# Kernel tuning notes

Hardware: AMD Instinct MI355X
Metric: run time of the kernel (lower is better)

The kernel has to match this reference:

```python
import jax, jax.numpy as jnp
import numpy as np

B, N, C = 2048, 49, 768
MID = 48  # 768 // 16
SELECT_SIZES = (36, 24)  # int(49*0.75), int(49*0.5)
LN_EPS = 1e-5


def _hier_se(x, w1, b1, w2, b2):
    """HierarchicalSE: SE gating + importance scores. x: [B, N, C]."""
    s = x.mean(axis=1)  # [B, C]
    h = jax.nn.gelu(s @ w1 + b1, approximate=False)
    gates = jax.nn.sigmoid(h @ w2 + b2)[:, None, :]  # [B, 1, C]
    out = x * gates
    ts = jnp.linalg.norm(out, axis=-1)  # [B, N]
    ts = ts - ts.mean(axis=-1, keepdims=True)
    std = jnp.std(ts, axis=-1, ddof=1, keepdims=True) + 1e-6  # torch std is unbiased
    importance = jax.nn.softmax(ts / std, axis=-1)
    return out, importance


def _select_patches(tokens, importance, k):
    _, idx = jax.lax.top_k(importance, k)  # [B, k]
    return jnp.take_along_axis(tokens, idx[:, :, None], axis=1)  # [B, k, C]


def setup_inputs() -> dict:
    key = jax.random.key(0)
    ks = jax.random.split(key, 8)
    sc = 0.02
    return {
        "x": jax.random.normal(ks[0], (B, N, C), dtype=jnp.float32),
        "se1_w1": jax.random.normal(ks[1], (C, MID), dtype=jnp.float32) * sc,
        "se1_b1": jnp.zeros((MID,), jnp.float32),
        "se1_w2": jax.random.normal(ks[2], (MID, C), dtype=jnp.float32) * sc,
        "se1_b2": jnp.zeros((C,), jnp.float32),
        "se2_w1": jax.random.normal(ks[3], (C, MID), dtype=jnp.float32) * sc,
        "se2_b1": jnp.zeros((MID,), jnp.float32),
        "se2_w2": jax.random.normal(ks[4], (MID, C), dtype=jnp.float32) * sc,
        "se2_b2": jnp.zeros((C,), jnp.float32),
        "ln_gamma": jnp.ones((C,), jnp.float32),
        "ln_beta": jnp.zeros((C,), jnp.float32),
        "cls_w": jax.random.normal(ks[5], (C, 5), dtype=jnp.float32) * sc,
        "cls_b": jnp.zeros((5,), jnp.float32),
    }


def reference(x, se1_w1, se1_b1, se1_w2, se1_b2,
              se2_w1, se2_b1, se2_w2, se2_b2,
              ln_gamma, ln_beta, cls_w, cls_b):
    tokens = x
    params = ((se1_w1, se1_b1, se1_w2, se1_b2), (se2_w1, se2_b1, se2_w2, se2_b2))
    for (w1, b1, w2, b2), k in zip(params, SELECT_SIZES):
        tokens_attn, importance = _hier_se(tokens, w1, b1, w2, b2)
        tokens = _select_patches(tokens_attn, importance, k)
    pooled = tokens.mean(axis=1)  # [B, C]
    mu = pooled.mean(axis=-1, keepdims=True)
    var = pooled.var(axis=-1, keepdims=True)
    normed = (pooled - mu) * jax.lax.rsqrt(var + LN_EPS) * ln_gamma + ln_beta
    return normed @ cls_w + cls_b  # [B, 5]
```

## Files before the change

kernel.cpp:

```cpp
#include <hip/hip_runtime.h>
#include <math.h>

#define NB    2048
#define NTOK  49
#define CH    768
#define MID   48
#define K1    36
#define K2    24
#define NU1   (NTOK - K1)
#define NU2   (K1 - K2)
#define NTHR  384

__device__ __forceinline__ float wsum(float v) {
    #pragma unroll
    for (int off = 32; off; off >>= 1) v += __shfl_xor(v, off, 64);
    return v;
}
__device__ __forceinline__ float gelu_exact(float v) {
    return 0.5f * v * (1.0f + erff(v * 0.70710678118654752440f));
}
__device__ __forceinline__ float sigmoidf(float v) {
    return 1.0f / (1.0f + expf(-v));
}

__global__ __launch_bounds__(NTHR, 6)
void fused_all(const float* __restrict__ x,
               const float* __restrict__ w1a, const float* __restrict__ b1a,
               const float* __restrict__ w2a, const float* __restrict__ b2a,
               const float* __restrict__ w1b, const float* __restrict__ b1b,
               const float* __restrict__ w2b, const float* __restrict__ b2b,
               const float* __restrict__ lng, const float* __restrict__ lnb,
               const float* __restrict__ cw,  const float* __restrict__ cb,
               float* __restrict__ out)
{
    __shared__ float colsum[CH];
    __shared__ float sA[CH];
    __shared__ float gv[CH];
    __shared__ float red[8 * MID];
    __shared__ float hb[MID];
    __shared__ float ts[64];
    __shared__ int   sel1[K1];
    __shared__ int   unsel1[NU1];
    __shared__ int   unsel2[NU2];
    __shared__ float scal[2];

    const int tid  = threadIdx.x;
    const int lane = tid & 63;
    const int wv   = tid >> 6;
    const int b    = blockIdx.x;
    const float* xb = x + (size_t)b * (NTOK * CH);

    {
        const float2* p = (const float2*)xb;
        float sx = 0.f, sy = 0.f;
        #pragma unroll 7
        for (int n = 0; n < NTOK; ++n) {
            float2 v = p[n * 384 + tid];
            sx += v.x; sy += v.y;
        }
        colsum[2*tid]   = sx;
        colsum[2*tid+1] = sy;
    }
    __syncthreads();

    {
        const int m = tid % MID, ch = tid / MID;
        const float* wp = w1a + (ch * 96) * MID + m;
        const float* sp = colsum + ch * 96;
        float a = 0.f;
        #pragma unroll
        for (int k = 0; k < 96; ++k) a = fmaf(sp[k], wp[k * MID], a);
        red[ch * MID + m] = a;
    }
    __syncthreads();
    if (tid < MID) {
        float v = 0.f;
        #pragma unroll
        for (int c = 0; c < 8; ++c) v += red[c * MID + tid];
        hb[tid] = gelu_exact(v * (1.0f / NTOK) + b1a[tid]);
    }
    __syncthreads();

    {
        const float2* w2r = (const float2*)w2a;
        float2 bb = ((const float2*)b2a)[tid];
        float a0 = bb.x, a1 = bb.y;
        #pragma unroll
        for (int m = 0; m < MID; ++m) {
            float2 w = w2r[(size_t)m * 384 + tid];
            float h = hb[m];
            a0 = fmaf(h, w.x, a0);
            a1 = fmaf(h, w.y, a1);
        }
        gv[2*tid]   = sigmoidf(a0);
        gv[2*tid+1] = sigmoidf(a1);
    }
    __syncthreads();

    {
        float gs[12];
        #pragma unroll
        for (int k = 0; k < 3; ++k) {
            float4 q = *(const float4*)&gv[4*lane + 256*k];
            gs[4*k+0] = q.x*q.x; gs[4*k+1] = q.y*q.y;
            gs[4*k+2] = q.z*q.z; gs[4*k+3] = q.w*q.w;
        }
        for (int n = wv; n < NTOK; n += 6) {
            const float4* row = (const float4*)(xb + n * CH);
            float acc = 0.f;
            #pragma unroll
            for (int k = 0; k < 3; ++k) {
                float4 v = row[lane + 64*k];
                acc = fmaf(v.x*v.x, gs[4*k+0], acc);
                acc = fmaf(v.y*v.y, gs[4*k+1], acc);
                acc = fmaf(v.z*v.z, gs[4*k+2], acc);
                acc = fmaf(v.w*v.w, gs[4*k+3], acc);
            }
            acc = wsum(acc);
            if (lane == 0) ts[n] = sqrtf(acc);
        }
    }
    __syncthreads();

    if (wv == 0) {
        float vl = (lane < NTOK) ? ts[lane] : -1.0f;
        int rank = 0;
        for (int j = 0; j < NTOK; ++j) {
            float vj = ts[j];
            rank += (vj > vl) || (vj == vl && j < lane);
        }
        if (lane < NTOK) {
            if (rank < K1) sel1[rank] = lane;
            else           unsel1[rank - K1] = lane;
        }
    }
    __syncthreads();

    {
        int rows[NU1];
        #pragma unroll
        for (int r = 0; r < NU1; ++r) rows[r] = unsel1[r] * CH;
        float2 cs = *(float2*)&colsum[2*tid];
        #pragma unroll
        for (int r = 0; r < NU1; ++r) {
            float2 v = *(const float2*)(xb + rows[r] + 2*tid);
            cs.x -= v.x; cs.y -= v.y;
        }
        *(float2*)&colsum[2*tid] = cs;
        float2 g = *(float2*)&gv[2*tid];
        sA[2*tid]   = cs.x * (1.0f / K1) * g.x;
        sA[2*tid+1] = cs.y * (1.0f / K1) * g.y;
    }
    __syncthreads();

    {
        const int m = tid % MID, ch = tid / MID;
        const float* wp = w1b + (ch * 96) * MID + m;
        const float* sp = sA + ch * 96;
        float a = 0.f;
        #pragma unroll
        for (int k = 0; k < 96; ++k) a = fmaf(sp[k], wp[k * MID], a);
        red[ch * MID + m] = a;
    }
    __syncthreads();
    if (tid < MID) {
        float v = 0.f;
        #pragma unroll
        for (int c = 0; c < 8; ++c) v += red[c * MID + tid];
        hb[tid] = gelu_exact(v + b1b[tid]);
    }
    __syncthreads();

    {
        const float2* w2r = (const float2*)w2b;
        float2 bb = ((const float2*)b2b)[tid];
        float a0 = bb.x, a1 = bb.y;
        #pragma unroll
        for (int m = 0; m < MID; ++m) {
            float2 w = w2r[(size_t)m * 384 + tid];
            float h = hb[m];
            a0 = fmaf(h, w.x, a0);
            a1 = fmaf(h, w.y, a1);
        }
        gv[2*tid]   *= sigmoidf(a0);
        gv[2*tid+1] *= sigmoidf(a1);
    }
    __syncthreads();

    {
        float gr[12];
        #pragma unroll
        for (int k = 0; k < 3; ++k) {
            float4 q = *(const float4*)&gv[4*lane + 256*k];
            gr[4*k+0] = q.x*q.x; gr[4*k+1] = q.y*q.y;
            gr[4*k+2] = q.z*q.z; gr[4*k+3] = q.w*q.w;
        }
        for (int j = wv; j < K1; j += 6) {
            const float4* row = (const float4*)(xb + sel1[j] * CH);
            float acc = 0.f;
            #pragma unroll
            for (int k = 0; k < 3; ++k) {
                float4 v = row[lane + 64*k];
                acc = fmaf(v.x*v.x, gr[4*k+0], acc);
                acc = fmaf(v.y*v.y, gr[4*k+1], acc);
                acc = fmaf(v.z*v.z, gr[4*k+2], acc);
                acc = fmaf(v.w*v.w, gr[4*k+3], acc);
            }
            acc = wsum(acc);
            if (lane == 0) ts[j] = sqrtf(acc);
        }
    }
    __syncthreads();

    if (wv == 0) {
        float vl = (lane < K1) ? ts[lane] : -1.0f;
        int rank = 0;
        for (int j = 0; j < K1; ++j) {
            float vj = ts[j];
            rank += (vj > vl) || (vj == vl && j < lane);
        }
        if (lane < K1 && rank >= K2) unsel2[rank - K2] = sel1[lane];
    }
    __syncthreads();

    {
        int rows[NU2];
        #pragma unroll
        for (int r = 0; r < NU2; ++r) rows[r] = unsel2[r] * CH;
        float2 cs = *(float2*)&colsum[2*tid];
        #pragma unroll
        for (int r = 0; r < NU2; ++r) {
            float2 v = *(const float2*)(xb + rows[r] + 2*tid);
            cs.x -= v.x; cs.y -= v.y;
        }
        float2 g = *(float2*)&gv[2*tid];
        sA[2*tid]   = cs.x * (1.0f / K2) * g.x;
        sA[2*tid+1] = cs.y * (1.0f / K2) * g.y;
    }
    __syncthreads();

    if (wv == 0) {
        float s = 0.f, q = 0.f;
        #pragma unroll
        for (int k = 0; k < CH/64; ++k) {
            float v = sA[lane + 64*k];
            s += v; q = fmaf(v, v, q);
        }
        s = wsum(s); q = wsum(q);
        if (lane == 0) {
            float mu  = s * (1.0f / CH);
            float var = q * (1.0f / CH) - mu * mu;
            scal[0] = mu;
            scal[1] = rsqrtf(var + 1e-5f);
        }
    }
    __syncthreads();

    if (wv < 5) {
        const float mu = scal[0], inv = scal[1];
        float acc = 0.f;
        #pragma unroll
        for (int k = 0; k < CH/64; ++k) {
            int c = lane + 64*k;
            float nv = (sA[c] - mu) * inv * lng[c] + lnb[c];
            acc = fmaf(nv, cw[c*5 + wv], acc);
        }
        acc = wsum(acc);
        if (lane == 0) out[(size_t)b*5 + wv] = acc + cb[wv];
    }
}

extern "C" void kernel_launch(void* const* d_in, const int* in_sizes, int n_in,
                              void* d_out, int out_size, void* d_ws, size_t ws_size,
                              hipStream_t stream) {
    (void)in_sizes; (void)n_in; (void)out_size; (void)d_ws; (void)ws_size;
    const float* x   = (const float*)d_in[0];
    const float* w1a = (const float*)d_in[1];
    const float* b1a = (const float*)d_in[2];
    const float* w2a = (const float*)d_in[3];
    const float* b2a = (const float*)d_in[4];
    const float* w1b = (const float*)d_in[5];
    const float* b1b = (const float*)d_in[6];
    const float* w2b = (const float*)d_in[7];
    const float* b2b = (const float*)d_in[8];
    const float* lng = (const float*)d_in[9];
    const float* lnb = (const float*)d_in[10];
    const float* cw  = (const float*)d_in[11];
    const float* cb  = (const float*)d_in[12];
    float* out = (float*)d_out;

    hipLaunchKernelGGL(fused_all, dim3(NB), dim3(NTHR), 0, stream,
                       x, w1a, b1a, w2a, b2a, w1b, b1b, w2b, b2b,
                       lng, lnb, cw, cb, out);
}
```

Before: 546.0 us.

## Process two batch rows per block to share SE weight loads

Each block now handles two batch elements instead of one. The SE MLP weight reads (w1, w2) are shared across both rows, and the reduction and top-k phases for the two rows run on separate waves. This halves the block count to 1024 and lowers the launch-bounds occupancy target from 6 to 4, which reduces latency hiding for the memory-bound x streaming while cutting redundant weight traffic and per-block sync overhead.

Measured after the change: 527.3 us. -3.4%, faster.

```diff
diff --git a/kernel.cpp b/kernel.cpp
--- a/kernel.cpp
+++ b/kernel.cpp
@@ -10,6 +10,7 @@
 #define NU1   (NTOK - K1)
 #define NU2   (K1 - K2)
 #define NTHR  384
+#define BPB   2
 
 __device__ __forceinline__ float wsum(float v) {
     #pragma unroll
@@ -23,85 +24,98 @@
     return 1.0f / (1.0f + expf(-v));
 }
 
-__global__ __launch_bounds__(NTHR, 6)
-void fused_all(const float* __restrict__ x,
-               const float* __restrict__ w1a, const float* __restrict__ b1a,
-               const float* __restrict__ w2a, const float* __restrict__ b2a,
-               const float* __restrict__ w1b, const float* __restrict__ b1b,
-               const float* __restrict__ w2b, const float* __restrict__ b2b,
-               const float* __restrict__ lng, const float* __restrict__ lnb,
-               const float* __restrict__ cw,  const float* __restrict__ cb,
-               float* __restrict__ out)
+__global__ __launch_bounds__(NTHR, 4)
+void fused2(const float* __restrict__ x,
+            const float* __restrict__ w1a, const float* __restrict__ b1a,
+            const float* __restrict__ w2a, const float* __restrict__ b2a,
+            const float* __restrict__ w1b, const float* __restrict__ b1b,
+            const float* __restrict__ w2b, const float* __restrict__ b2b,
+            const float* __restrict__ lng, const float* __restrict__ lnb,
+            const float* __restrict__ cw,  const float* __restrict__ cb,
+            float* __restrict__ out)
 {
-    __shared__ float colsum[CH];
-    __shared__ float sA[CH];
-    __shared__ float gv[CH];
-    __shared__ float red[8 * MID];
-    __shared__ float hb[MID];
-    __shared__ float ts[64];
-    __shared__ int   sel1[K1];
-    __shared__ int   unsel1[NU1];
-    __shared__ int   unsel2[NU2];
-    __shared__ float scal[2];
+    __shared__ float colsum[BPB][CH];
+    __shared__ float sA[BPB][CH];
+    __shared__ float gv[BPB][CH];
+    __shared__ float red[BPB][8*MID];
+    __shared__ float hb[BPB][MID];
+    __shared__ float ts[BPB][64];
+    __shared__ int   sel1[BPB][K1];
+    __shared__ int   unsel1[BPB][NU1];
+    __shared__ int   unsel2[BPB][NU2];
+    __shared__ float scal[BPB][2];
 
     const int tid  = threadIdx.x;
     const int lane = tid & 63;
     const int wv   = tid >> 6;
-    const int b    = blockIdx.x;
-    const float* xb = x + (size_t)b * (NTOK * CH);
-
-    {
-        const float2* p = (const float2*)xb;
-        float sx = 0.f, sy = 0.f;
+    const int b0   = blockIdx.x * BPB;
+    const float* xb0 = x + (size_t)b0 * (NTOK * CH);
+    const float* xb1 = xb0 + (NTOK * CH);
+
+    {
+        const float2* pa = (const float2*)xb0;
+        const float2* pb = (const float2*)xb1;
+        float ax = 0.f, ay = 0.f, bx = 0.f, by = 0.f;
         #pragma unroll 7
         for (int n = 0; n < NTOK; ++n) {
-            float2 v = p[n * 384 + tid];
-            sx += v.x; sy += v.y;
-        }
-        colsum[2*tid]   = sx;
-        colsum[2*tid+1] = sy;
+            float2 va = pa[n * 384 + tid];
+            float2 vb = pb[n * 384 + tid];
+            ax += va.x; ay += va.y;
+            bx += vb.x; by += vb.y;
+        }
+        colsum[0][2*tid] = ax; colsum[0][2*tid+1] = ay;
+        colsum[1][2*tid] = bx; colsum[1][2*tid+1] = by;
     }
     __syncthreads();
 
     {
         const int m = tid % MID, ch = tid / MID;
         const float* wp = w1a + (ch * 96) * MID + m;
-        const float* sp = colsum + ch * 96;
-        float a = 0.f;
-        #pragma unroll
-        for (int k = 0; k < 96; ++k) a = fmaf(sp[k], wp[k * MID], a);
-        red[ch * MID + m] = a;
-    }
-    __syncthreads();
-    if (tid < MID) {
+        const float* s0 = &colsum[0][ch * 96];
+        const float* s1 = &colsum[1][ch * 96];
+        float a0 = 0.f, a1 = 0.f;
+        #pragma unroll
+        for (int k = 0; k < 96; ++k) {
+            float w = wp[k * MID];
+            a0 = fmaf(s0[k], w, a0);
+            a1 = fmaf(s1[k], w, a1);
+        }
+        red[0][ch * MID + m] = a0;
+        red[1][ch * MID + m] = a1;
+    }
+    __syncthreads();
+    if (tid < BPB * MID) {
+        const int bi = tid / MID, m = tid % MID;
         float v = 0.f;
         #pragma unroll
-        for (int c = 0; c < 8; ++c) v += red[c * MID + tid];
-        hb[tid] = gelu_exact(v * (1.0f / NTOK) + b1a[tid]);
+        for (int c = 0; c < 8; ++c) v += red[bi][c * MID + m];
+        hb[bi][m] = gelu_exact(v * (1.0f / NTOK) + b1a[m]);
     }
     __syncthreads();
 
     {
         const float2* w2r = (const float2*)w2a;
         float2 bb = ((const float2*)b2a)[tid];
-        float a0 = bb.x, a1 = bb.y;
+        float a0x = bb.x, a0y = bb.y, a1x = bb.x, a1y = bb.y;
         #pragma unroll
         for (int m = 0; m < MID; ++m) {
             float2 w = w2r[(size_t)m * 384 + tid];
-            float h = hb[m];
-            a0 = fmaf(h, w.x, a0);
-            a1 = fmaf(h, w.y, a1);
-        }
-        gv[2*tid]   = sigmoidf(a0);
-        gv[2*tid+1] = sigmoidf(a1);
-    }
-    __syncthreads();
-
-    {
+            float h0 = hb[0][m], h1 = hb[1][m];
+            a0x = fmaf(h0, w.x, a0x); a0y = fmaf(h0, w.y, a0y);
+            a1x = fmaf(h1, w.x, a1x); a1y = fmaf(h1, w.y, a1y);
+        }
+        gv[0][2*tid] = sigmoidf(a0x); gv[0][2*tid+1] = sigmoidf(a0y);
+        gv[1][2*tid] = sigmoidf(a1x); gv[1][2*tid+1] = sigmoidf(a1y);
+    }
+    __syncthreads();
+
+    #pragma unroll
+    for (int bi = 0; bi < BPB; ++bi) {
+        const float* xb = bi ? xb1 : xb0;
         float gs[12];
         #pragma unroll
         for (int k = 0; k < 3; ++k) {
-            float4 q = *(const float4*)&gv[4*lane + 256*k];
+            float4 q = *(const float4*)&gv[bi][4*lane + 256*k];
             gs[4*k+0] = q.x*q.x; gs[4*k+1] = q.y*q.y;
             gs[4*k+2] = q.z*q.z; gs[4*k+3] = q.w*q.w;
         }
@@ -117,86 +131,98 @@
                 acc = fmaf(v.w*v.w, gs[4*k+3], acc);
             }
             acc = wsum(acc);
-            if (lane == 0) ts[n] = sqrtf(acc);
-        }
-    }
-    __syncthreads();
-
-    if (wv == 0) {
-        float vl = (lane < NTOK) ? ts[lane] : -1.0f;
+            if (lane == 0) ts[bi][n] = sqrtf(acc);
+        }
+    }
+    __syncthreads();
+
+    if (wv < BPB) {
+        const int bi = wv;
+        float vl = (lane < NTOK) ? ts[bi][lane] : -1.0f;
         int rank = 0;
         for (int j = 0; j < NTOK; ++j) {
-            float vj = ts[j];
+            float vj = ts[bi][j];
             rank += (vj > vl) || (vj == vl && j < lane);
         }
         if (lane < NTOK) {
-            if (rank < K1) sel1[rank] = lane;
-            else           unsel1[rank - K1] = lane;
-        }
-    }
-    __syncthreads();
-
-    {
+            if (rank < K1) sel1[bi][rank] = lane;
+            else           unsel1[bi][rank - K1] = lane;
+        }
+    }
+    __syncthreads();
+
+    #pragma unroll
+    for (int bi = 0; bi < BPB; ++bi) {
+        const float* xb = bi ? xb1 : xb0;
         int rows[NU1];
         #pragma unroll
-        for (int r = 0; r < NU1; ++r) rows[r] = unsel1[r] * CH;
-        float2 cs = *(float2*)&colsum[2*tid];
+        for (int r = 0; r < NU1; ++r) rows[r] = unsel1[bi][r] * CH;
+        float2 cs = *(float2*)&colsum[bi][2*tid];
         #pragma unroll
         for (int r = 0; r < NU1; ++r) {
             float2 v = *(const float2*)(xb + rows[r] + 2*tid);
             cs.x -= v.x; cs.y -= v.y;
         }
-        *(float2*)&colsum[2*tid] = cs;
-        float2 g = *(float2*)&gv[2*tid];
-        sA[2*tid]   = cs.x * (1.0f / K1) * g.x;
-        sA[2*tid+1] = cs.y * (1.0f / K1) * g.y;
+        *(float2*)&colsum[bi][2*tid] = cs;
+        float2 g = *(float2*)&gv[bi][2*tid];
+        sA[bi][2*tid]   = cs.x * (1.0f / K1) * g.x;
+        sA[bi][2*tid+1] = cs.y * (1.0f / K1) * g.y;
     }
     __syncthreads();
 
     {
         const int m = tid % MID, ch = tid / MID;
         const float* wp = w1b + (ch * 96) * MID + m;
-        const float* sp = sA + ch * 96;
-        float a = 0.f;
-        #pragma unroll
-        for (int k = 0; k < 96; ++k) a = fmaf(sp[k], wp[k * MID], a);
-        red[ch * MID + m] = a;
-    }
-    __syncthreads();
-    if (tid < MID) {
+        const float* s0 = &sA[0][ch * 96];
+        const float* s1 = &sA[1][ch * 96];
+        float a0 = 0.f, a1 = 0.f;
+        #pragma unroll
+        for (int k = 0; k < 96; ++k) {
+            float w = wp[k * MID];
+            a0 = fmaf(s0[k], w, a0);
+            a1 = fmaf(s1[k], w, a1);
+        }
+        red[0][ch * MID + m] = a0;
+        red[1][ch * MID + m] = a1;
+    }
+    __syncthreads();
+    if (tid < BPB * MID) {
+        const int bi = tid / MID, m = tid % MID;
         float v = 0.f;
         #pragma unroll
-        for (int c = 0; c < 8; ++c) v += red[c * MID + tid];
-        hb[tid] = gelu_exact(v + b1b[tid]);
+        for (int c = 0; c < 8; ++c) v += red[bi][c * MID + m];
+        hb[bi][m] = gelu_exact(v + b1b[m]);
     }
     __syncthreads();
 
     {
         const float2* w2r = (const float2*)w2b;
         float2 bb = ((const float2*)b2b)[tid];
-        float a0 = bb.x, a1 = bb.y;
+        float a0x = bb.x, a0y = bb.y, a1x = bb.x, a1y = bb.y;
         #pragma unroll
         for (int m = 0; m < MID; ++m) {
             float2 w = w2r[(size_t)m * 384 + tid];
-            float h = hb[m];
-            a0 = fmaf(h, w.x, a0);
-            a1 = fmaf(h, w.y, a1);
-        }
-        gv[2*tid]   *= sigmoidf(a0);
-        gv[2*tid+1] *= sigmoidf(a1);
-    }
-    __syncthreads();
-
-    {
+            float h0 = hb[0][m], h1 = hb[1][m];
+            a0x = fmaf(h0, w.x, a0x); a0y = fmaf(h0, w.y, a0y);
+            a1x = fmaf(h1, w.x, a1x); a1y = fmaf(h1, w.y, a1y);
+        }
+        gv[0][2*tid]   *= sigmoidf(a0x); gv[0][2*tid+1] *= sigmoidf(a0y);
+        gv[1][2*tid]   *= sigmoidf(a1x); gv[1][2*tid+1] *= sigmoidf(a1y);
+    }
+    __syncthreads();
+
+    #pragma unroll
+    for (int bi = 0; bi < BPB; ++bi) {
+        const float* xb = bi ? xb1 : xb0;
         float gr[12];
         #pragma unroll
         for (int k = 0; k < 3; ++k) {
-            float4 q = *(const float4*)&gv[4*lane + 256*k];
+            float4 q = *(const float4*)&gv[bi][4*lane + 256*k];
             gr[4*k+0] = q.x*q.x; gr[4*k+1] = q.y*q.y;
             gr[4*k+2] = q.z*q.z; gr[4*k+3] = q.w*q.w;
         }
         for (int j = wv; j < K1; j += 6) {
-            const float4* row = (const float4*)(xb + sel1[j] * CH);
+            const float4* row = (const float4*)(xb + sel1[bi][j] * CH);
             float acc = 0.f;
             #pragma unroll
             for (int k = 0; k < 3; ++k) {
@@ -207,66 +233,71 @@
                 acc = fmaf(v.w*v.w, gr[4*k+3], acc);
             }
             acc = wsum(acc);
-            if (lane == 0) ts[j] = sqrtf(acc);
-        }
-    }
-    __syncthreads();
-
-    if (wv == 0) {
-        float vl = (lane < K1) ? ts[lane] : -1.0f;
+            if (lane == 0) ts[bi][j] = sqrtf(acc);
+        }
+    }
+    __syncthreads();
+
+    if (wv < BPB) {
+        const int bi = wv;
+        float vl = (lane < K1) ? ts[bi][lane] : -1.0f;
         int rank = 0;
         for (int j = 0; j < K1; ++j) {
-            float vj = ts[j];
+            float vj = ts[bi][j];
             rank += (vj > vl) || (vj == vl && j < lane);
         }
-        if (lane < K1 && rank >= K2) unsel2[rank - K2] = sel1[lane];
-    }
-    __syncthreads();
-
-    {
+        if (lane < K1 && rank >= K2) unsel2[bi][rank - K2] = sel1[bi][lane];
+    }
+    __syncthreads();
+
+    #pragma unroll
+    for (int bi = 0; bi < BPB; ++bi) {
+        const float* xb = bi ? xb1 : xb0;
         int rows[NU2];
         #pragma unroll
-        for (int r = 0; r < NU2; ++r) rows[r] = unsel2[r] * CH;
-        float2 cs = *(float2*)&colsum[2*tid];
+        for (int r = 0; r < NU2; ++r) rows[r] = unsel2[bi][r] * CH;
+        float2 cs = *(float2*)&colsum[bi][2*tid];
         #pragma unroll
         for (int r = 0; r < NU2; ++r) {
             float2 v = *(const float2*)(xb + rows[r] + 2*tid);
             cs.x -= v.x; cs.y -= v.y;
         }
-        float2 g = *(float2*)&gv[2*tid];
-        sA[2*tid]   = cs.x * (1.0f / K2) * g.x;
-        sA[2*tid+1] = cs.y * (1.0f / K2) * g.y;
-    }
-    __syncthreads();
-
-    if (wv == 0) {
+        float2 g = *(float2*)&gv[bi][2*tid];
+        sA[bi][2*tid]   = cs.x * (1.0f / K2) * g.x;
+        sA[bi][2*tid+1] = cs.y * (1.0f / K2) * g.y;
+    }
+    __syncthreads();
+
+    if (wv < BPB) {
+        const int bi = wv;
         float s = 0.f, q = 0.f;
         #pragma unroll
         for (int k = 0; k < CH/64; ++k) {
-            float v = sA[lane + 64*k];
+            float v = sA[bi][lane + 64*k];
             s += v; q = fmaf(v, v, q);
         }
         s = wsum(s); q = wsum(q);
         if (lane == 0) {
             float mu  = s * (1.0f / CH);
             float var = q * (1.0f / CH) - mu * mu;
-            scal[0] = mu;
-            scal[1] = rsqrtf(var + 1e-5f);
-        }
-    }
-    __syncthreads();
-
-    if (wv < 5) {
-        const float mu = scal[0], inv = scal[1];
+            scal[bi][0] = mu;
+            scal[bi][1] = rsqrtf(var + 1e-5f);
+        }
+    }
+    __syncthreads();
+
+    for (int t = wv; t < BPB * 5; t += 6) {
+        const int bi = t / 5, k5 = t % 5;
+        const float mu = scal[bi][0], inv = scal[bi][1];
         float acc = 0.f;
         #pragma unroll
         for (int k = 0; k < CH/64; ++k) {
             int c = lane + 64*k;
-            float nv = (sA[c] - mu) * inv * lng[c] + lnb[c];
-            acc = fmaf(nv, cw[c*5 + wv], acc);
+            float nv = (sA[bi][c] - mu) * inv * lng[c] + lnb[c];
+            acc = fmaf(nv, cw[c*5 + k5], acc);
         }
         acc = wsum(acc);
-        if (lane == 0) out[(size_t)b*5 + wv] = acc + cb[wv];
+        if (lane == 0) out[(size_t)(b0 + bi)*5 + k5] = acc + cb[k5];
     }
 }
 
@@ -289,7 +320,7 @@
     const float* cb  = (const float*)d_in[12];
     float* out = (float*)d_out;
 
-    hipLaunchKernelGGL(fused_all, dim3(NB), dim3(NTHR), 0, stream,
+    hipLaunchKernelGGL(fused2, dim3(NB / BPB), dim3(NTHR), 0, stream,
                        x, w1a, b1a, w2a, b2a, w1b, b1b, w2b, b2b,
                        lng, lnb, cw, cb, out);
 }
```
